# Kernel optimization log

Hardware: AMD Instinct MI355X
Metric: run time of the kernel (lower is better)

## Reference

```python
import jax, jax.numpy as jnp
import numpy as np

CHANNELS = 768
N_HEADS = 12
HEAD_DIM = CHANNELS // N_HEADS
WINDOW = 4
B, T = 4, 1024


def setup_inputs() -> dict:
    key = jax.random.key(0)
    ks = jax.random.split(key, 11)
    C = CHANNELS
    s = 1.0 / np.sqrt(C)
    inp = {
        "x": jax.random.normal(ks[0], (B, C, T), dtype=jnp.float32),
        "w_q": jax.random.normal(ks[1], (C, C), dtype=jnp.float32) * s,
        "b_q": jnp.zeros((C,), dtype=jnp.float32),
        "w_k": jax.random.normal(ks[2], (C, C), dtype=jnp.float32) * s,
        "b_k": jnp.zeros((C,), dtype=jnp.float32),
        "w_v": jax.random.normal(ks[3], (C, C), dtype=jnp.float32) * s,
        "b_v": jnp.zeros((C,), dtype=jnp.float32),
        "w_o": jax.random.normal(ks[4], (C, C), dtype=jnp.float32) * s,
        "b_o": jnp.zeros((C,), dtype=jnp.float32),
        "emb_rel_k": jax.random.normal(ks[5], (2 * WINDOW + 1, HEAD_DIM), dtype=jnp.float32) * 0.01,
        "emb_rel_v": jax.random.normal(ks[6], (2 * WINDOW + 1, HEAD_DIM), dtype=jnp.float32) * 0.01,
    }
    return inp


def _rel_embeddings(emb_k, emb_v, t):
    pos = jnp.arange(t)
    rel_pos = pos[None, :] - pos[:, None]            # (T, T), rel_pos[i,j] = j - i
    outside = jnp.abs(rel_pos) > WINDOW
    rel_idx = jnp.clip(rel_pos, -WINDOW, WINDOW) + WINDOW
    rel_k = jnp.where(outside[:, :, None], 0.0, emb_k[rel_idx])  # (T, T, d)
    rel_v = jnp.where(outside[:, :, None], 0.0, emb_v[rel_idx])
    return rel_k, rel_v


def reference(x, w_q, b_q, w_k, b_k, w_v, b_v, w_o, b_o, emb_rel_k, emb_rel_v):
    Bq, C, t = x.shape
    H, d = N_HEADS, HEAD_DIM
    # 1x1 Conv1d == per-timestep linear over channels
    def proj(w, b):
        return jnp.einsum('oc,bct->bot', w, x) + b[None, :, None]
    # (B, C, T) -> (B, H, T, d)
    def split_heads(y):
        return y.reshape(Bq, H, d, t).transpose(0, 1, 3, 2)
    q = split_heads(proj(w_q, b_q)) / jnp.sqrt(jnp.float32(d))
    k = split_heads(proj(w_k, b_k))
    v = split_heads(proj(w_v, b_v))
    scores = jnp.einsum('bhid,bhjd->bhij', q, k)
    rel_k, rel_v = _rel_embeddings(emb_rel_k, emb_rel_v, t)
    scores = scores + jnp.einsum('bhid,ijd->bhij', q, rel_k)
    attn = jax.nn.softmax(scores, axis=-1)
    out = jnp.einsum('bhij,bhjd->bhid', attn, v)
    out = out + jnp.einsum('bhij,ijd->bhid', attn, rel_v)
    out = out.transpose(0, 1, 3, 2).reshape(Bq, C, t)  # (B, C, T)
    out = jnp.einsum('oc,bct->bot', w_o, out) + b_o[None, :, None]
    return out
```

## Files before the change

### kernel.cpp

```cpp
#include <hip/hip_runtime.h>

#define B_ 4
#define T_ 1024
#define C_ 768
#define H_ 12
#define D_ 64

typedef unsigned short u16;
typedef __attribute__((ext_vector_type(8))) short b16x8;
typedef __attribute__((ext_vector_type(4))) float f32x4;

#define MFMA(a, b, c) __builtin_amdgcn_mfma_f32_16x16x32_bf16(a, b, c, 0, 0, 0)

__device__ __forceinline__ float b2f(u16 u) {
    return __uint_as_float(((unsigned)u) << 16);
}
__device__ __forceinline__ u16 f2b(float f) {
    unsigned u = __float_as_uint(f);
    u += 0x7fffu + ((u >> 16) & 1u);
    return (u16)(u >> 16);
}
__device__ __forceinline__ u16 f2b_tr(float f) {
    return (u16)(__float_as_uint(f) >> 16);
}

__device__ __forceinline__ void g2l16(const u16* g, u16* l) {
    __builtin_amdgcn_global_load_lds(
        (const __attribute__((address_space(1))) unsigned int*)g,
        (__attribute__((address_space(3))) unsigned int*)l, 16, 0, 0);
}

__global__ __launch_bounds__(256) void convw_kernel(
    const float* __restrict__ w0, const float* __restrict__ w1,
    const float* __restrict__ w2, const float* __restrict__ w3,
    u16* __restrict__ o)
{
    const float* src = blockIdx.y == 0 ? w0 : blockIdx.y == 1 ? w1 :
                       blockIdx.y == 2 ? w2 : w3;
    u16* dst = o + (size_t)blockIdx.y * C_ * C_;
    const int i = (blockIdx.x * 256 + threadIdx.x) * 4;
    float4 v = *(const float4*)(src + i);
    ushort4 st = {f2b(v.x), f2b(v.y), f2b(v.z), f2b(v.w)};
    *(ushort4*)(dst + i) = st;
}

__global__ __launch_bounds__(256) void convx_kernel(
    const float* __restrict__ x, u16* __restrict__ xb)
{
    __shared__ u16 tile[64][68];
    const int tid = threadIdx.x;
    const int t0 = blockIdx.x * 64, c0 = blockIdx.y * 64, b = blockIdx.z;
    #pragma unroll
    for (int p = 0; p < 4; ++p) {
        const int cc = p * 16 + (tid >> 4);
        const int t4 = (tid & 15) * 4;
        float4 v = *(const float4*)(x + ((size_t)b * C_ + c0 + cc) * T_ + t0 + t4);
        tile[t4 + 0][cc] = f2b(v.x);
        tile[t4 + 1][cc] = f2b(v.y);
        tile[t4 + 2][cc] = f2b(v.z);
        tile[t4 + 3][cc] = f2b(v.w);
    }
    __syncthreads();
    #pragma unroll
    for (int p = 0; p < 4; ++p) {
        const int tt = p * 16 + (tid >> 4);
        const int c4 = (tid & 15) * 4;
        ushort4 st = *(const ushort4*)&tile[tt][c4];
        *(ushort4*)(xb + ((size_t)b * T_ + t0 + tt) * C_ + c0 + c4) = st;
    }
}

__global__ __launch_bounds__(256) void qkv_mfma_kernel(
    const u16* __restrict__ wb, const u16* __restrict__ xb,
    const float* __restrict__ b_q, const float* __restrict__ b_k,
    const float* __restrict__ b_v,
    u16* __restrict__ q_ws, u16* __restrict__ k_ws, u16* __restrict__ v_ws)
{
    __shared__ __align__(16) u16 a_s[128 * 32];
    __shared__ __align__(16) u16 b_s[128 * 32];

    const int tid = threadIdx.x;
    const int wv = tid >> 6, lane = tid & 63;
    const int lo = lane & 15, quad = lane >> 4;
    const int wm = wv >> 1, wn = wv & 1;
    const int swz = (lo >> 1) & 3;
    const int srow = lane >> 2;
    const int skb  = (lane & 3) ^ ((lane >> 3) & 3);

    const int t0 = blockIdx.x * 128;
    const int mat = blockIdx.y / 6, oy = blockIdx.y % 6;
    const int o0 = oy * 128;
    const int b  = blockIdx.z;

    const u16* A = wb + (size_t)mat * C_ * C_;
    const float* bias = mat == 0 ? b_q : (mat == 1 ? b_k : b_v);
    u16* dst = mat == 0 ? q_ws : (mat == 1 ? k_ws : v_ws);
    const float scale = mat == 0 ? 0.125f : 1.0f;

    const size_t bT0 = (size_t)b * T_ + t0;

    f32x4 acc[4][4] = {};

    for (int kk = 0; kk < C_; kk += 32) {
        __syncthreads();
        #pragma unroll
        for (int ia = 0; ia < 2; ++ia) {
            const int row0 = (wv * 2 + ia) * 16;
            g2l16(A + (size_t)(o0 + row0 + srow) * C_ + kk + skb * 8,
                  a_s + row0 * 32);
        }
        #pragma unroll
        for (int ib = 0; ib < 2; ++ib) {
            const int row0 = (wv * 2 + ib) * 16;
            g2l16(xb + (bT0 + row0 + srow) * C_ + kk + skb * 8,
                  b_s + row0 * 32);
        }
        __syncthreads();

        b16x8 af[4], bf[4];
        #pragma unroll
        for (int mi = 0; mi < 4; ++mi) {
            const int m = wm * 64 + mi * 16 + lo;
            af[mi] = *(const b16x8*)(a_s + m * 32 + (quad ^ swz) * 8);
        }
        #pragma unroll
        for (int ni = 0; ni < 4; ++ni) {
            const int n = wn * 64 + ni * 16 + lo;
            bf[ni] = *(const b16x8*)(b_s + n * 32 + (quad ^ swz) * 8);
        }
        #pragma unroll
        for (int mi = 0; mi < 4; ++mi)
            #pragma unroll
            for (int ni = 0; ni < 4; ++ni)
                acc[mi][ni] = MFMA(af[mi], bf[ni], acc[mi][ni]);
    }

    #pragma unroll
    for (int mi = 0; mi < 4; ++mi) {
        const int o_b = o0 + wm * 64 + mi * 16 + quad * 4;
        const float4 bv4 = *(const float4*)(bias + o_b);
        const int h = o_b >> 6;
        const int dd0 = o_b & 63;
        #pragma unroll
        for (int ni = 0; ni < 4; ++ni) {
            const int t = t0 + wn * 64 + ni * 16 + lo;
            f32x4 a = acc[mi][ni];
            ushort4 st;
            st.x = f2b((a[0] + bv4.x) * scale);
            st.y = f2b((a[1] + bv4.y) * scale);
            st.z = f2b((a[2] + bv4.z) * scale);
            st.w = f2b((a[3] + bv4.w) * scale);
            *(ushort4*)(dst + (((size_t)b * H_ + h) * T_ + t) * D_ + dd0) = st;
        }
    }
}

__global__ __launch_bounds__(256) void transv_kernel(
    const u16* __restrict__ src, u16* __restrict__ dst)
{
    __shared__ __align__(16) u16 tile[64 * 72];
    const int tid = threadIdx.x;
    const int t0 = blockIdx.x * 64;
    const int bh = blockIdx.y;
    const u16* s = src + (size_t)bh * T_ * D_;
    u16* d = dst + (size_t)bh * D_ * T_;
    #pragma unroll
    for (int p = 0; p < 2; ++p) {
        const int idx = tid + p * 256;
        const int row = idx >> 3, ch = idx & 7;
        *(b16x8*)(tile + row * 72 + ch * 8) =
            *(const b16x8*)(s + (size_t)(t0 + row) * D_ + ch * 8);
    }
    __syncthreads();
    #pragma unroll
    for (int p = 0; p < 2; ++p) {
        const int idx = tid + p * 256;
        const int dd = idx >> 3, ch = idx & 7;
        union { b16x8 v; u16 e[8]; } t;
        #pragma unroll
        for (int e = 0; e < 8; ++e)
            t.e[e] = tile[(ch * 8 + e) * 72 + dd];
        *(b16x8*)(d + (size_t)dd * T_ + t0 + ch * 8) = t.v;
    }
}

__global__ __launch_bounds__(256) void out_mfma_kernel(
    const u16* __restrict__ wob, const u16* __restrict__ ab,
    const float* __restrict__ bias, float* __restrict__ out)
{
    __shared__ __align__(16) u16 a_s[64 * 32];
    __shared__ __align__(16) u16 b_s[128 * 32];

    const int tid = threadIdx.x;
    const int wv = tid >> 6, lane = tid & 63;
    const int lo = lane & 15, quad = lane >> 4;
    const int wm = wv >> 1, wn = wv & 1;
    const int swz = (lo >> 1) & 3;
    const int srow = lane >> 2;
    const int skb  = (lane & 3) ^ ((lane >> 3) & 3);

    const int t0 = blockIdx.x * 128;
    const int o0 = blockIdx.y * 64;
    const int b  = blockIdx.z;
    const size_t bT0 = (size_t)b * T_ + t0;

    f32x4 acc[2][4] = {};

    for (int kk = 0; kk < C_; kk += 32) {
        __syncthreads();
        {
            const int row0 = wv * 16;
            g2l16(wob + (size_t)(o0 + row0 + srow) * C_ + kk + skb * 8,
                  a_s + row0 * 32);
        }
        #pragma unroll
        for (int ib = 0; ib < 2; ++ib) {
            const int row0 = (wv * 2 + ib) * 16;
            g2l16(ab + (bT0 + row0 + srow) * C_ + kk + skb * 8,
                  b_s + row0 * 32);
        }
        __syncthreads();

        b16x8 af[2], bf[4];
        #pragma unroll
        for (int mi = 0; mi < 2; ++mi) {
            const int m = wm * 32 + mi * 16 + lo;
            af[mi] = *(const b16x8*)(a_s + m * 32 + (quad ^ swz) * 8);
        }
        #pragma unroll
        for (int ni = 0; ni < 4; ++ni) {
            const int n = wn * 64 + ni * 16 + lo;
            bf[ni] = *(const b16x8*)(b_s + n * 32 + (quad ^ swz) * 8);
        }
        #pragma unroll
        for (int mi = 0; mi < 2; ++mi)
            #pragma unroll
            for (int ni = 0; ni < 4; ++ni)
                acc[mi][ni] = MFMA(af[mi], bf[ni], acc[mi][ni]);
    }

    #pragma unroll
    for (int mi = 0; mi < 2; ++mi) {
        const int o_b = o0 + wm * 32 + mi * 16 + quad * 4;
        const float4 bv4 = *(const float4*)(bias + o_b);
        const float bb[4] = {bv4.x, bv4.y, bv4.z, bv4.w};
        #pragma unroll
        for (int ni = 0; ni < 4; ++ni) {
            const int t = t0 + wn * 64 + ni * 16 + lo;
            f32x4 a = acc[mi][ni];
            #pragma unroll
            for (int r = 0; r < 4; ++r)
                out[((size_t)b * C_ + o_b + r) * T_ + t] = a[r] + bb[r];
        }
    }
}

__global__ __launch_bounds__(256, 2) void attn_mfma_kernel(
    const u16* __restrict__ qw, const u16* __restrict__ kw, const u16* __restrict__ vw,
    const float* __restrict__ erk, const float* __restrict__ erv,
    u16* __restrict__ att)
{
    __shared__ __align__(16) u16 k_s[64 * 64];
    __shared__ __align__(16) u16 v_s[64 * 64];
    __shared__ __align__(16) u16 p_s[64 * 64];
    __shared__ float qrel_s[64][9];
    __shared__ float band_s[64][9];
    __shared__ float alpha_s[64];

    const int tid = threadIdx.x;
    const int wv = tid >> 6, lane = tid & 63;
    const int lo = lane & 15, quad = lane >> 4;
    const int wi0 = wv * 16;
    const int it0 = blockIdx.x * 64;
    const int h = blockIdx.y, b = blockIdx.z;
    const int bh = b * H_ + h;

    const u16* qp = qw + (size_t)bh * T_ * D_;
    const u16* kp = kw + (size_t)bh * T_ * D_;
    const u16* vp = vw + (size_t)bh * D_ * T_;

    const int srow = lane >> 3;
    const int schunk = (lane & 7) ^ (srow & 7);
    const int lsw = lo & 7;

    b16x8 qf[2];
    #pragma unroll
    for (int kc = 0; kc < 2; ++kc)
        qf[kc] = *(const b16x8*)(qp + (size_t)(it0 + wi0 + lo) * D_ + kc * 32 + quad * 8);

    {
        b16x8 ekf[2];
        #pragma unroll
        for (int kc = 0; kc < 2; ++kc) {
            union { b16x8 v; u16 s[8]; } t;
            #pragma unroll
            for (int r = 0; r < 8; ++r) t.s[r] = 0;
            if (lo < 9) {
                const float* e = erk + lo * D_ + kc * 32 + quad * 8;
                #pragma unroll
                for (int r = 0; r < 8; ++r) t.s[r] = f2b(e[r]);
            }
            ekf[kc] = t.v;
        }
        f32x4 acc = {};
        acc = MFMA(qf[0], ekf[0], acc);
        acc = MFMA(qf[1], ekf[1], acc);
        if (lo < 9)
            #pragma unroll
            for (int r = 0; r < 4; ++r)
                qrel_s[wi0 + quad * 4 + r][lo] = acc[r];
    }

    for (int idx = lane; idx < 16 * 9; idx += 64)
        band_s[wi0 + idx / 9][idx % 9] = -1e30f;

    f32x4 o[4] = {};
    float m = -1e30f, l = 0.f;

    for (int jt = 0; jt < T_; jt += 64) {
        __syncthreads();
        #pragma unroll
        for (int i2 = 0; i2 < 2; ++i2) {
            const int row0 = (wv * 2 + i2) * 8;
            g2l16(kp + (size_t)(jt + row0 + srow) * D_ + schunk * 8, k_s + row0 * 64);
            g2l16(vp + (size_t)(row0 + srow) * T_ + jt + schunk * 8, v_s + row0 * 64);
        }
        __syncthreads();

        f32x4 st[4];
        #pragma unroll
        for (int mt = 0; mt < 4; ++mt) {
            const int kr = mt * 16 + lo;
            const b16x8 ka0 = *(const b16x8*)(k_s + kr * 64 + ((quad) ^ lsw) * 8);
            const b16x8 ka1 = *(const b16x8*)(k_s + kr * 64 + ((4 + quad) ^ lsw) * 8);
            f32x4 a = {};
            a = MFMA(ka0, qf[0], a);
            a = MFMA(ka1, qf[1], a);
            st[mt] = a;
        }

        const int ibase = it0 + wi0 + lo;
        #pragma unroll
        for (int mt = 0; mt < 4; ++mt)
            #pragma unroll
            for (int r = 0; r < 4; ++r) {
                const int rr = (jt + mt * 16 + quad * 4 + r) - ibase + 4;
                if (rr >= 0 && rr <= 8) {
                    const float s2 = st[mt][r] + qrel_s[wi0 + lo][rr];
                    st[mt][r] = s2;
                    band_s[wi0 + lo][rr] = s2;
                }
            }

        float tm = -1e30f;
        #pragma unroll
        for (int mt = 0; mt < 4; ++mt)
            #pragma unroll
            for (int r = 0; r < 4; ++r)
                tm = fmaxf(tm, st[mt][r]);
        tm = fmaxf(tm, __shfl_xor(tm, 16));
        tm = fmaxf(tm, __shfl_xor(tm, 32));
        const float nm = fmaxf(m, tm);
        const float al = __expf(m - nm);
        m = nm;
        float rs = 0.f;
        #pragma unroll
        for (int mt = 0; mt < 4; ++mt)
            #pragma unroll
            for (int r = 0; r < 4; ++r) {
                const float e = __expf(st[mt][r] - nm);
                st[mt][r] = e;
                rs += e;
            }
        rs += __shfl_xor(rs, 16);
        rs += __shfl_xor(rs, 32);
        l = l * al + rs;
        if (quad == 0) alpha_s[wi0 + lo] = al;

        #pragma unroll
        for (int mt = 0; mt < 4; ++mt) {
            ushort4 pw;
            pw.x = f2b_tr(st[mt][0]);
            pw.y = f2b_tr(st[mt][1]);
            pw.z = f2b_tr(st[mt][2]);
            pw.w = f2b_tr(st[mt][3]);
            const int slot = (mt * 2 + (quad >> 1)) ^ lsw;
            *(ushort4*)(p_s + (wi0 + lo) * 64 + slot * 8 + (quad & 1) * 4) = pw;
        }

        #pragma unroll
        for (int r = 0; r < 4; ++r) {
            const float a = alpha_s[wi0 + quad * 4 + r];
            #pragma unroll
            for (int nd = 0; nd < 4; ++nd)
                o[nd][r] *= a;
        }

        const b16x8 pa0 = *(const b16x8*)(p_s + (wi0 + lo) * 64 + ((quad) ^ lsw) * 8);
        const b16x8 pa1 = *(const b16x8*)(p_s + (wi0 + lo) * 64 + ((4 + quad) ^ lsw) * 8);
        #pragma unroll
        for (int nd = 0; nd < 4; ++nd) {
            const int vr = nd * 16 + lo;
            const b16x8 vb0 = *(const b16x8*)(v_s + vr * 64 + ((quad) ^ lsw) * 8);
            const b16x8 vb1 = *(const b16x8*)(v_s + vr * 64 + ((4 + quad) ^ lsw) * 8);
            o[nd] = MFMA(pa0, vb0, o[nd]);
            o[nd] = MFMA(pa1, vb1, o[nd]);
        }
    }

    {
        union { b16x8 v; u16 s[8]; } tb;
        #pragma unroll
        for (int r = 0; r < 8; ++r) {
            const int rr = quad * 8 + r;
            tb.s[r] = (rr <= 8) ? f2b(__expf(band_s[wi0 + lo][rr] - m)) : (u16)0;
        }
        const b16x8 baf = tb.v;
        #pragma unroll
        for (int nd = 0; nd < 4; ++nd) {
            union { b16x8 v; u16 s[8]; } t;
            #pragma unroll
            for (int r = 0; r < 8; ++r) {
                const int rr = quad * 8 + r;
                t.s[r] = (rr <= 8) ? f2b(erv[rr * D_ + nd * 16 + lo]) : (u16)0;
            }
            o[nd] = MFMA(baf, t.v, o[nd]);
        }
    }

    if (quad == 0) alpha_s[wi0 + lo] = 1.f / l;
    #pragma unroll
    for (int r = 0; r < 4; ++r) {
        const int il = wi0 + quad * 4 + r;
        const float inv = alpha_s[il];
        const size_t base = ((size_t)b * T_ + it0 + il) * C_ + h * D_;
        #pragma unroll
        for (int nd = 0; nd < 4; ++nd)
            att[base + nd * 16 + lo] = f2b(o[nd][r] * inv);
    }
}

extern "C" void kernel_launch(void* const* d_in, const int* in_sizes, int n_in,
                              void* d_out, int out_size, void* d_ws, size_t ws_size,
                              hipStream_t stream) {
    const float* x   = (const float*)d_in[0];
    const float* w_q = (const float*)d_in[1];
    const float* b_q = (const float*)d_in[2];
    const float* w_k = (const float*)d_in[3];
    const float* b_k = (const float*)d_in[4];
    const float* w_v = (const float*)d_in[5];
    const float* b_v = (const float*)d_in[6];
    const float* w_o = (const float*)d_in[7];
    const float* b_o = (const float*)d_in[8];
    const float* erk = (const float*)d_in[9];
    const float* erv = (const float*)d_in[10];

    const size_t N = (size_t)B_ * C_ * T_;
    u16* q_ws  = (u16*)d_ws;
    u16* k_ws  = q_ws + N;
    u16* vraw  = q_ws + 2 * N;
    u16* vdT   = q_ws + 3 * N;
    u16* xb    = q_ws + 4 * N;
    u16* a_ws  = vraw;
    u16* wb    = q_ws + 5 * N;
    float* out = (float*)d_out;

    dim3 blk(256, 1, 1);

    convw_kernel<<<dim3(C_ * C_ / 1024, 4), blk, 0, stream>>>(w_q, w_k, w_v, w_o, wb);
    convx_kernel<<<dim3(T_ / 64, C_ / 64, B_), blk, 0, stream>>>(x, xb);

    qkv_mfma_kernel<<<dim3(T_ / 128, 18, B_), blk, 0, stream>>>(
        wb, xb, b_q, b_k, b_v, q_ws, k_ws, vraw);

    transv_kernel<<<dim3(T_ / 64, H_ * B_), blk, 0, stream>>>(vraw, vdT);

    attn_mfma_kernel<<<dim3(T_ / 64, H_, B_), blk, 0, stream>>>(
        q_ws, k_ws, vdT, erk, erv, a_ws);

    out_mfma_kernel<<<dim3(T_ / 128, C_ / 64, B_), blk, 0, stream>>>(
        wb + 3 * (size_t)C_ * C_, a_ws, b_o, out);
}
```

Baseline: 174.6 us.

## Double GEMM K-tile depth and shrink attention blocks to 32 query rows

The QKV and output projection GEMMs now stage 64-wide K slices per iteration instead of 32, using an 8-chunk XOR swizzle. This halves the number of barrier-separated load phases and runs two MFMA K-steps per sync. The attention kernel now uses 128-thread blocks covering 32 query rows, which doubles the grid to improve occupancy and load balance. It also skips the relative-position band loop for key tiles that cannot overlap the window. The cost is more shared memory per GEMM block and K/V tiles loaded twice as often across attention blocks.

New measurement: 172.4 us. Within noise of the previous version (-1.2%).

```diff
diff --git a/kernel.cpp b/kernel.cpp
--- a/kernel.cpp
+++ b/kernel.cpp
@@ -76,16 +76,16 @@
     const float* __restrict__ b_v,
     u16* __restrict__ q_ws, u16* __restrict__ k_ws, u16* __restrict__ v_ws)
 {
-    __shared__ __align__(16) u16 a_s[128 * 32];
-    __shared__ __align__(16) u16 b_s[128 * 32];
+    __shared__ __align__(16) u16 a_s[128 * 64];
+    __shared__ __align__(16) u16 b_s[128 * 64];
 
     const int tid = threadIdx.x;
     const int wv = tid >> 6, lane = tid & 63;
     const int lo = lane & 15, quad = lane >> 4;
     const int wm = wv >> 1, wn = wv & 1;
-    const int swz = (lo >> 1) & 3;
-    const int srow = lane >> 2;
-    const int skb  = (lane & 3) ^ ((lane >> 3) & 3);
+    const int lsw = lo & 7;
+    const int srow = lane >> 3;
+    const int schunk = (lane & 7) ^ srow;
 
     const int t0 = blockIdx.x * 128;
     const int mat = blockIdx.y / 6, oy = blockIdx.y % 6;
@@ -101,38 +101,42 @@
 
     f32x4 acc[4][4] = {};
 
-    for (int kk = 0; kk < C_; kk += 32) {
-        __syncthreads();
-        #pragma unroll
-        for (int ia = 0; ia < 2; ++ia) {
-            const int row0 = (wv * 2 + ia) * 16;
-            g2l16(A + (size_t)(o0 + row0 + srow) * C_ + kk + skb * 8,
-                  a_s + row0 * 32);
-        }
-        #pragma unroll
-        for (int ib = 0; ib < 2; ++ib) {
-            const int row0 = (wv * 2 + ib) * 16;
-            g2l16(xb + (bT0 + row0 + srow) * C_ + kk + skb * 8,
-                  b_s + row0 * 32);
-        }
-        __syncthreads();
-
-        b16x8 af[4], bf[4];
-        #pragma unroll
-        for (int mi = 0; mi < 4; ++mi) {
-            const int m = wm * 64 + mi * 16 + lo;
-            af[mi] = *(const b16x8*)(a_s + m * 32 + (quad ^ swz) * 8);
-        }
-        #pragma unroll
-        for (int ni = 0; ni < 4; ++ni) {
-            const int n = wn * 64 + ni * 16 + lo;
-            bf[ni] = *(const b16x8*)(b_s + n * 32 + (quad ^ swz) * 8);
-        }
-        #pragma unroll
-        for (int mi = 0; mi < 4; ++mi)
-            #pragma unroll
-            for (int ni = 0; ni < 4; ++ni)
-                acc[mi][ni] = MFMA(af[mi], bf[ni], acc[mi][ni]);
+    for (int kk = 0; kk < C_; kk += 64) {
+        __syncthreads();
+        #pragma unroll
+        for (int ia = 0; ia < 4; ++ia) {
+            const int row0 = (wv * 4 + ia) * 8;
+            g2l16(A + (size_t)(o0 + row0 + srow) * C_ + kk + schunk * 8,
+                  a_s + row0 * 64);
+        }
+        #pragma unroll
+        for (int ib = 0; ib < 4; ++ib) {
+            const int row0 = (wv * 4 + ib) * 8;
+            g2l16(xb + (bT0 + row0 + srow) * C_ + kk + schunk * 8,
+                  b_s + row0 * 64);
+        }
+        __syncthreads();
+
+        #pragma unroll
+        for (int kc = 0; kc < 2; ++kc) {
+            const int slotk = kc * 4;
+            b16x8 af[4], bf[4];
+            #pragma unroll
+            for (int mi = 0; mi < 4; ++mi) {
+                const int m = wm * 64 + mi * 16 + lo;
+                af[mi] = *(const b16x8*)(a_s + m * 64 + ((slotk + quad) ^ lsw) * 8);
+            }
+            #pragma unroll
+            for (int ni = 0; ni < 4; ++ni) {
+                const int n = wn * 64 + ni * 16 + lo;
+                bf[ni] = *(const b16x8*)(b_s + n * 64 + ((slotk + quad) ^ lsw) * 8);
+            }
+            #pragma unroll
+            for (int mi = 0; mi < 4; ++mi)
+                #pragma unroll
+                for (int ni = 0; ni < 4; ++ni)
+                    acc[mi][ni] = MFMA(af[mi], bf[ni], acc[mi][ni]);
+        }
     }
 
     #pragma unroll
@@ -188,16 +192,16 @@
     const u16* __restrict__ wob, const u16* __restrict__ ab,
     const float* __restrict__ bias, float* __restrict__ out)
 {
-    __shared__ __align__(16) u16 a_s[64 * 32];
-    __shared__ __align__(16) u16 b_s[128 * 32];
+    __shared__ __align__(16) u16 a_s[64 * 64];
+    __shared__ __align__(16) u16 b_s[128 * 64];
 
     const int tid = threadIdx.x;
     const int wv = tid >> 6, lane = tid & 63;
     const int lo = lane & 15, quad = lane >> 4;
     const int wm = wv >> 1, wn = wv & 1;
-    const int swz = (lo >> 1) & 3;
-    const int srow = lane >> 2;
-    const int skb  = (lane & 3) ^ ((lane >> 3) & 3);
+    const int lsw = lo & 7;
+    const int srow = lane >> 3;
+    const int schunk = (lane & 7) ^ srow;
 
     const int t0 = blockIdx.x * 128;
     const int o0 = blockIdx.y * 64;
@@ -206,37 +210,42 @@
 
     f32x4 acc[2][4] = {};
 
-    for (int kk = 0; kk < C_; kk += 32) {
-        __syncthreads();
-        {
-            const int row0 = wv * 16;
-            g2l16(wob + (size_t)(o0 + row0 + srow) * C_ + kk + skb * 8,
-                  a_s + row0 * 32);
-        }
-        #pragma unroll
-        for (int ib = 0; ib < 2; ++ib) {
-            const int row0 = (wv * 2 + ib) * 16;
-            g2l16(ab + (bT0 + row0 + srow) * C_ + kk + skb * 8,
-                  b_s + row0 * 32);
-        }
-        __syncthreads();
-
-        b16x8 af[2], bf[4];
-        #pragma unroll
-        for (int mi = 0; mi < 2; ++mi) {
-            const int m = wm * 32 + mi * 16 + lo;
-            af[mi] = *(const b16x8*)(a_s + m * 32 + (quad ^ swz) * 8);
-        }
-        #pragma unroll
-        for (int ni = 0; ni < 4; ++ni) {
-            const int n = wn * 64 + ni * 16 + lo;
-            bf[ni] = *(const b16x8*)(b_s + n * 32 + (quad ^ swz) * 8);
-        }
-        #pragma unroll
-        for (int mi = 0; mi < 2; ++mi)
-            #pragma unroll
-            for (int ni = 0; ni < 4; ++ni)
-                acc[mi][ni] = MFMA(af[mi], bf[ni], acc[mi][ni]);
+    for (int kk = 0; kk < C_; kk += 64) {
+        __syncthreads();
+        #pragma unroll
+        for (int ia = 0; ia < 2; ++ia) {
+            const int row0 = (wv * 2 + ia) * 8;
+            g2l16(wob + (size_t)(o0 + row0 + srow) * C_ + kk + schunk * 8,
+                  a_s + row0 * 64);
+        }
+        #pragma unroll
+        for (int ib = 0; ib < 4; ++ib) {
+            const int row0 = (wv * 4 + ib) * 8;
+            g2l16(ab + (bT0 + row0 + srow) * C_ + kk + schunk * 8,
+                  b_s + row0 * 64);
+        }
+        __syncthreads();
+
+        #pragma unroll
+        for (int kc = 0; kc < 2; ++kc) {
+            const int slotk = kc * 4;
+            b16x8 af[2], bf[4];
+            #pragma unroll
+            for (int mi = 0; mi < 2; ++mi) {
+                const int m = wm * 32 + mi * 16 + lo;
+                af[mi] = *(const b16x8*)(a_s + m * 64 + ((slotk + quad) ^ lsw) * 8);
+            }
+            #pragma unroll
+            for (int ni = 0; ni < 4; ++ni) {
+                const int n = wn * 64 + ni * 16 + lo;
+                bf[ni] = *(const b16x8*)(b_s + n * 64 + ((slotk + quad) ^ lsw) * 8);
+            }
+            #pragma unroll
+            for (int mi = 0; mi < 2; ++mi)
+                #pragma unroll
+                for (int ni = 0; ni < 4; ++ni)
+                    acc[mi][ni] = MFMA(af[mi], bf[ni], acc[mi][ni]);
+        }
     }
 
     #pragma unroll
@@ -255,23 +264,23 @@
     }
 }
 
-__global__ __launch_bounds__(256, 2) void attn_mfma_kernel(
+__global__ __launch_bounds__(128, 4) void attn_mfma_kernel(
     const u16* __restrict__ qw, const u16* __restrict__ kw, const u16* __restrict__ vw,
     const float* __restrict__ erk, const float* __restrict__ erv,
     u16* __restrict__ att)
 {
     __shared__ __align__(16) u16 k_s[64 * 64];
     __shared__ __align__(16) u16 v_s[64 * 64];
-    __shared__ __align__(16) u16 p_s[64 * 64];
-    __shared__ float qrel_s[64][9];
-    __shared__ float band_s[64][9];
-    __shared__ float alpha_s[64];
+    __shared__ __align__(16) u16 p_s[32 * 64];
+    __shared__ float qrel_s[32][9];
+    __shared__ float band_s[32][9];
+    __shared__ float alpha_s[32];
 
     const int tid = threadIdx.x;
     const int wv = tid >> 6, lane = tid & 63;
     const int lo = lane & 15, quad = lane >> 4;
     const int wi0 = wv * 16;
-    const int it0 = blockIdx.x * 64;
+    const int it0 = blockIdx.x * 32;
     const int h = blockIdx.y, b = blockIdx.z;
     const int bh = b * H_ + h;
 
@@ -280,7 +289,7 @@
     const u16* vp = vw + (size_t)bh * D_ * T_;
 
     const int srow = lane >> 3;
-    const int schunk = (lane & 7) ^ (srow & 7);
+    const int schunk = (lane & 7) ^ srow;
     const int lsw = lo & 7;
 
     b16x8 qf[2];
@@ -320,8 +329,8 @@
     for (int jt = 0; jt < T_; jt += 64) {
         __syncthreads();
         #pragma unroll
-        for (int i2 = 0; i2 < 2; ++i2) {
-            const int row0 = (wv * 2 + i2) * 8;
+        for (int i2 = 0; i2 < 4; ++i2) {
+            const int row0 = (wv * 4 + i2) * 8;
             g2l16(kp + (size_t)(jt + row0 + srow) * D_ + schunk * 8, k_s + row0 * 64);
             g2l16(vp + (size_t)(row0 + srow) * T_ + jt + schunk * 8, v_s + row0 * 64);
         }
@@ -339,18 +348,20 @@
             st[mt] = a;
         }
 
-        const int ibase = it0 + wi0 + lo;
-        #pragma unroll
-        for (int mt = 0; mt < 4; ++mt)
-            #pragma unroll
-            for (int r = 0; r < 4; ++r) {
-                const int rr = (jt + mt * 16 + quad * 4 + r) - ibase + 4;
-                if (rr >= 0 && rr <= 8) {
-                    const float s2 = st[mt][r] + qrel_s[wi0 + lo][rr];
-                    st[mt][r] = s2;
-                    band_s[wi0 + lo][rr] = s2;
+        if (jt >= it0 - 67 && jt <= it0 + 35) {
+            const int ibase = it0 + wi0 + lo;
+            #pragma unroll
+            for (int mt = 0; mt < 4; ++mt)
+                #pragma unroll
+                for (int r = 0; r < 4; ++r) {
+                    const int rr = (jt + mt * 16 + quad * 4 + r) - ibase + 4;
+                    if (rr >= 0 && rr <= 8) {
+                        const float s2 = st[mt][r] + qrel_s[wi0 + lo][rr];
+                        st[mt][r] = s2;
+                        band_s[wi0 + lo][rr] = s2;
+                    }
                 }
-            }
+        }
 
         float tm = -1e30f;
         #pragma unroll
@@ -475,7 +486,7 @@
 
     transv_kernel<<<dim3(T_ / 64, H_ * B_), blk, 0, stream>>>(vraw, vdT);
 
-    attn_mfma_kernel<<<dim3(T_ / 64, H_, B_), blk, 0, stream>>>(
+    attn_mfma_kernel<<<dim3(T_ / 32, H_, B_), dim3(128, 1, 1), 0, stream>>>(
         q_ws, k_ws, vdT, erk, erv, a_ws);
 
     out_mfma_kernel<<<dim3(T_ / 128, C_ / 64, B_), blk, 0, stream>>>(
```

## Process two query row-tiles per wave in attention, halving waves per block

Applied to the files above, without the earlier changes.

The attention kernel now runs 2 waves of 128 threads per block, each wave handling 32 query rows (two 16-row tiles), so the K and V fragments loaded from LDS are reused across two MFMA tiles. Each wave issues twice as many global-to-LDS loads per key tile. The relative-position band update is now skipped for key tiles far from the query block. The cost is more registers per wave and fewer waves available to hide latency.

After: 178.6 us. 1.02x slower.

```diff
diff --git a/kernel.cpp b/kernel.cpp
--- a/kernel.cpp
+++ b/kernel.cpp
@@ -255,7 +255,7 @@
     }
 }
 
-__global__ __launch_bounds__(256, 2) void attn_mfma_kernel(
+__global__ __launch_bounds__(128, 2) void attn_mfma_kernel(
     const u16* __restrict__ qw, const u16* __restrict__ kw, const u16* __restrict__ vw,
     const float* __restrict__ erk, const float* __restrict__ erv,
     u16* __restrict__ att)
@@ -270,7 +270,7 @@
     const int tid = threadIdx.x;
     const int wv = tid >> 6, lane = tid & 63;
     const int lo = lane & 15, quad = lane >> 4;
-    const int wi0 = wv * 16;
+    const int wi0 = wv * 32;
     const int it0 = blockIdx.x * 64;
     const int h = blockIdx.y, b = blockIdx.z;
     const int bh = b * H_ + h;
@@ -280,13 +280,16 @@
     const u16* vp = vw + (size_t)bh * D_ * T_;
 
     const int srow = lane >> 3;
-    const int schunk = (lane & 7) ^ (srow & 7);
+    const int schunk = (lane & 7) ^ srow;
     const int lsw = lo & 7;
 
-    b16x8 qf[2];
-    #pragma unroll
-    for (int kc = 0; kc < 2; ++kc)
-        qf[kc] = *(const b16x8*)(qp + (size_t)(it0 + wi0 + lo) * D_ + kc * 32 + quad * 8);
+    b16x8 qf[2][2];
+    #pragma unroll
+    for (int it = 0; it < 2; ++it)
+        #pragma unroll
+        for (int kc = 0; kc < 2; ++kc)
+            qf[it][kc] = *(const b16x8*)(
+                qp + (size_t)(it0 + wi0 + it * 16 + lo) * D_ + kc * 32 + quad * 8);
 
     {
         b16x8 ekf[2];
@@ -302,120 +305,155 @@
             }
             ekf[kc] = t.v;
         }
-        f32x4 acc = {};
-        acc = MFMA(qf[0], ekf[0], acc);
-        acc = MFMA(qf[1], ekf[1], acc);
-        if (lo < 9)
-            #pragma unroll
-            for (int r = 0; r < 4; ++r)
-                qrel_s[wi0 + quad * 4 + r][lo] = acc[r];
-    }
-
-    for (int idx = lane; idx < 16 * 9; idx += 64)
+        #pragma unroll
+        for (int it = 0; it < 2; ++it) {
+            f32x4 acc = {};
+            acc = MFMA(qf[it][0], ekf[0], acc);
+            acc = MFMA(qf[it][1], ekf[1], acc);
+            if (lo < 9)
+                #pragma unroll
+                for (int r = 0; r < 4; ++r)
+                    qrel_s[wi0 + it * 16 + quad * 4 + r][lo] = acc[r];
+        }
+    }
+
+    for (int idx = lane; idx < 32 * 9; idx += 64)
         band_s[wi0 + idx / 9][idx % 9] = -1e30f;
 
-    f32x4 o[4] = {};
-    float m = -1e30f, l = 0.f;
+    f32x4 o[2][4] = {};
+    float m[2] = {-1e30f, -1e30f};
+    float l[2] = {0.f, 0.f};
 
     for (int jt = 0; jt < T_; jt += 64) {
         __syncthreads();
         #pragma unroll
-        for (int i2 = 0; i2 < 2; ++i2) {
-            const int row0 = (wv * 2 + i2) * 8;
+        for (int i2 = 0; i2 < 4; ++i2) {
+            const int row0 = (wv * 4 + i2) * 8;
             g2l16(kp + (size_t)(jt + row0 + srow) * D_ + schunk * 8, k_s + row0 * 64);
             g2l16(vp + (size_t)(row0 + srow) * T_ + jt + schunk * 8, v_s + row0 * 64);
         }
         __syncthreads();
 
-        f32x4 st[4];
+        f32x4 st[4][2];
         #pragma unroll
         for (int mt = 0; mt < 4; ++mt) {
             const int kr = mt * 16 + lo;
             const b16x8 ka0 = *(const b16x8*)(k_s + kr * 64 + ((quad) ^ lsw) * 8);
             const b16x8 ka1 = *(const b16x8*)(k_s + kr * 64 + ((4 + quad) ^ lsw) * 8);
-            f32x4 a = {};
-            a = MFMA(ka0, qf[0], a);
-            a = MFMA(ka1, qf[1], a);
-            st[mt] = a;
-        }
-
-        const int ibase = it0 + wi0 + lo;
-        #pragma unroll
-        for (int mt = 0; mt < 4; ++mt)
+            #pragma unroll
+            for (int it = 0; it < 2; ++it) {
+                f32x4 a = {};
+                a = MFMA(ka0, qf[it][0], a);
+                a = MFMA(ka1, qf[it][1], a);
+                st[mt][it] = a;
+            }
+        }
+
+        if (jt >= it0 - 67 && jt <= it0 + 67) {
+            #pragma unroll
+            for (int it = 0; it < 2; ++it) {
+                const int irow = wi0 + it * 16 + lo;
+                const int ibase = it0 + irow;
+                #pragma unroll
+                for (int mt = 0; mt < 4; ++mt)
+                    #pragma unroll
+                    for (int r = 0; r < 4; ++r) {
+                        const int rr = (jt + mt * 16 + quad * 4 + r) - ibase + 4;
+                        if (rr >= 0 && rr <= 8) {
+                            const float s2 = st[mt][it][r] + qrel_s[irow][rr];
+                            st[mt][it][r] = s2;
+                            band_s[irow][rr] = s2;
+                        }
+                    }
+            }
+        }
+
+        #pragma unroll
+        for (int it = 0; it < 2; ++it) {
+            float tm = -1e30f;
+            #pragma unroll
+            for (int mt = 0; mt < 4; ++mt)
+                #pragma unroll
+                for (int r = 0; r < 4; ++r)
+                    tm = fmaxf(tm, st[mt][it][r]);
+            tm = fmaxf(tm, __shfl_xor(tm, 16));
+            tm = fmaxf(tm, __shfl_xor(tm, 32));
+            const float nm = fmaxf(m[it], tm);
+            const float al = __expf(m[it] - nm);
+            m[it] = nm;
+            float rs = 0.f;
+            #pragma unroll
+            for (int mt = 0; mt < 4; ++mt)
+                #pragma unroll
+                for (int r = 0; r < 4; ++r) {
+                    const float e = __expf(st[mt][it][r] - nm);
+                    st[mt][it][r] = e;
+                    rs += e;
+                }
+            rs += __shfl_xor(rs, 16);
+            rs += __shfl_xor(rs, 32);
+            l[it] = l[it] * al + rs;
+            if (quad == 0) alpha_s[wi0 + it * 16 + lo] = al;
+        }
+
+        #pragma unroll
+        for (int it = 0; it < 2; ++it) {
+            const int rowp = wi0 + it * 16 + lo;
+            #pragma unroll
+            for (int mt = 0; mt < 4; ++mt) {
+                ushort4 pw;
+                pw.x = f2b_tr(st[mt][it][0]);
+                pw.y = f2b_tr(st[mt][it][1]);
+                pw.z = f2b_tr(st[mt][it][2]);
+                pw.w = f2b_tr(st[mt][it][3]);
+                const int slot = (mt * 2 + (quad >> 1)) ^ lsw;
+                *(ushort4*)(p_s + rowp * 64 + slot * 8 + (quad & 1) * 4) = pw;
+            }
+        }
+
+        #pragma unroll
+        for (int it = 0; it < 2; ++it)
             #pragma unroll
             for (int r = 0; r < 4; ++r) {
-                const int rr = (jt + mt * 16 + quad * 4 + r) - ibase + 4;
-                if (rr >= 0 && rr <= 8) {
-                    const float s2 = st[mt][r] + qrel_s[wi0 + lo][rr];
-                    st[mt][r] = s2;
-                    band_s[wi0 + lo][rr] = s2;
-                }
-            }
-
-        float tm = -1e30f;
-        #pragma unroll
-        for (int mt = 0; mt < 4; ++mt)
-            #pragma unroll
-            for (int r = 0; r < 4; ++r)
-                tm = fmaxf(tm, st[mt][r]);
-        tm = fmaxf(tm, __shfl_xor(tm, 16));
-        tm = fmaxf(tm, __shfl_xor(tm, 32));
-        const float nm = fmaxf(m, tm);
-        const float al = __expf(m - nm);
-        m = nm;
-        float rs = 0.f;
-        #pragma unroll
-        for (int mt = 0; mt < 4; ++mt)
-            #pragma unroll
-            for (int r = 0; r < 4; ++r) {
-                const float e = __expf(st[mt][r] - nm);
-                st[mt][r] = e;
-                rs += e;
-            }
-        rs += __shfl_xor(rs, 16);
-        rs += __shfl_xor(rs, 32);
-        l = l * al + rs;
-        if (quad == 0) alpha_s[wi0 + lo] = al;
-
-        #pragma unroll
-        for (int mt = 0; mt < 4; ++mt) {
-            ushort4 pw;
-            pw.x = f2b_tr(st[mt][0]);
-            pw.y = f2b_tr(st[mt][1]);
-            pw.z = f2b_tr(st[mt][2]);
-            pw.w = f2b_tr(st[mt][3]);
-            const int slot = (mt * 2 + (quad >> 1)) ^ lsw;
-            *(ushort4*)(p_s + (wi0 + lo) * 64 + slot * 8 + (quad & 1) * 4) = pw;
-        }
-
-        #pragma unroll
-        for (int r = 0; r < 4; ++r) {
-            const float a = alpha_s[wi0 + quad * 4 + r];
-            #pragma unroll
-            for (int nd = 0; nd < 4; ++nd)
-                o[nd][r] *= a;
-        }
-
-        const b16x8 pa0 = *(const b16x8*)(p_s + (wi0 + lo) * 64 + ((quad) ^ lsw) * 8);
-        const b16x8 pa1 = *(const b16x8*)(p_s + (wi0 + lo) * 64 + ((4 + quad) ^ lsw) * 8);
+                const float a = alpha_s[wi0 + it * 16 + quad * 4 + r];
+                #pragma unroll
+                for (int nd = 0; nd < 4; ++nd)
+                    o[it][nd][r] *= a;
+            }
+
+        b16x8 vb[4][2];
         #pragma unroll
         for (int nd = 0; nd < 4; ++nd) {
             const int vr = nd * 16 + lo;
-            const b16x8 vb0 = *(const b16x8*)(v_s + vr * 64 + ((quad) ^ lsw) * 8);
-            const b16x8 vb1 = *(const b16x8*)(v_s + vr * 64 + ((4 + quad) ^ lsw) * 8);
-            o[nd] = MFMA(pa0, vb0, o[nd]);
-            o[nd] = MFMA(pa1, vb1, o[nd]);
+            vb[nd][0] = *(const b16x8*)(v_s + vr * 64 + ((quad) ^ lsw) * 8);
+            vb[nd][1] = *(const b16x8*)(v_s + vr * 64 + ((4 + quad) ^ lsw) * 8);
+        }
+        #pragma unroll
+        for (int it = 0; it < 2; ++it) {
+            const int rowp = wi0 + it * 16 + lo;
+            const b16x8 pa0 = *(const b16x8*)(p_s + rowp * 64 + ((quad) ^ lsw) * 8);
+            const b16x8 pa1 = *(const b16x8*)(p_s + rowp * 64 + ((4 + quad) ^ lsw) * 8);
+            #pragma unroll
+            for (int nd = 0; nd < 4; ++nd) {
+                o[it][nd] = MFMA(pa0, vb[nd][0], o[it][nd]);
+                o[it][nd] = MFMA(pa1, vb[nd][1], o[it][nd]);
+            }
         }
     }
 
     {
-        union { b16x8 v; u16 s[8]; } tb;
-        #pragma unroll
-        for (int r = 0; r < 8; ++r) {
-            const int rr = quad * 8 + r;
-            tb.s[r] = (rr <= 8) ? f2b(__expf(band_s[wi0 + lo][rr] - m)) : (u16)0;
-        }
-        const b16x8 baf = tb.v;
+        b16x8 baf[2];
+        #pragma unroll
+        for (int it = 0; it < 2; ++it) {
+            union { b16x8 v; u16 s[8]; } tb;
+            #pragma unroll
+            for (int r = 0; r < 8; ++r) {
+                const int rr = quad * 8 + r;
+                tb.s[r] = (rr <= 8) ? f2b(__expf(band_s[wi0 + it * 16 + lo][rr] - m[it]))
+                                    : (u16)0;
+            }
+            baf[it] = tb.v;
+        }
         #pragma unroll
         for (int nd = 0; nd < 4; ++nd) {
             union { b16x8 v; u16 s[8]; } t;
@@ -424,20 +462,26 @@
                 const int rr = quad * 8 + r;
                 t.s[r] = (rr <= 8) ? f2b(erv[rr * D_ + nd * 16 + lo]) : (u16)0;
             }
-            o[nd] = MFMA(baf, t.v, o[nd]);
-        }
-    }
-
-    if (quad == 0) alpha_s[wi0 + lo] = 1.f / l;
-    #pragma unroll
-    for (int r = 0; r < 4; ++r) {
-        const int il = wi0 + quad * 4 + r;
-        const float inv = alpha_s[il];
-        const size_t base = ((size_t)b * T_ + it0 + il) * C_ + h * D_;
-        #pragma unroll
-        for (int nd = 0; nd < 4; ++nd)
-            att[base + nd * 16 + lo] = f2b(o[nd][r] * inv);
-    }
+            #pragma unroll
+            for (int it = 0; it < 2; ++it)
+                o[it][nd] = MFMA(baf[it], t.v, o[it][nd]);
+        }
+    }
+
+    #pragma unroll
+    for (int it = 0; it < 2; ++it)
+        if (quad == 0) alpha_s[wi0 + it * 16 + lo] = 1.f / l[it];
+    #pragma unroll
+    for (int it = 0; it < 2; ++it)
+        #pragma unroll
+        for (int r = 0; r < 4; ++r) {
+            const int il = wi0 + it * 16 + quad * 4 + r;
+            const float inv = alpha_s[il];
+            const size_t base = ((size_t)b * T_ + it0 + il) * C_ + h * D_;
+            #pragma unroll
+            for (int nd = 0; nd < 4; ++nd)
+                att[base + nd * 16 + lo] = f2b(o[it][nd][r] * inv);
+        }
 }
 
 extern "C" void kernel_launch(void* const* d_in, const int* in_sizes, int n_in,
@@ -475,7 +519,7 @@
 
     transv_kernel<<<dim3(T_ / 64, H_ * B_), blk, 0, stream>>>(vraw, vdT);
 
-    attn_mfma_kernel<<<dim3(T_ / 64, H_, B_), blk, 0, stream>>>(
+    attn_mfma_kernel<<<dim3(T_ / 64, H_, B_), dim3(128, 1, 1), 0, stream>>>(
         q_ws, k_ws, vdT, erk, erv, a_ws);
 
     out_mfma_kernel<<<dim3(T_ / 128, C_ / 64, B_), blk, 0, stream>>>(
```

## Widen attention key tile to 128 and skip band work outside window

Applied to the files above, without the earlier changes.

The flash-attention loop now processes 128 keys per iteration instead of 64. This halves the number of barrier and softmax-rescale rounds, and the K/V/P shared buffers grow to match with a 16-chunk XOR swizzle. The relative-position band update is now skipped for key tiles that cannot intersect the window. In exchange it uses more LDS and registers (st[8]), which may reduce occupancy under launch_bounds(256,2).

After: 184.9 us. +5.9%, slower.

```diff
diff --git a/kernel.cpp b/kernel.cpp
--- a/kernel.cpp
+++ b/kernel.cpp
@@ -260,9 +260,9 @@
     const float* __restrict__ erk, const float* __restrict__ erv,
     u16* __restrict__ att)
 {
-    __shared__ __align__(16) u16 k_s[64 * 64];
-    __shared__ __align__(16) u16 v_s[64 * 64];
-    __shared__ __align__(16) u16 p_s[64 * 64];
+    __shared__ __align__(16) u16 k_s[128 * 64];
+    __shared__ __align__(16) u16 v_s[64 * 128];
+    __shared__ __align__(16) u16 p_s[64 * 128];
     __shared__ float qrel_s[64][9];
     __shared__ float band_s[64][9];
     __shared__ float alpha_s[64];
@@ -279,9 +279,10 @@
     const u16* kp = kw + (size_t)bh * T_ * D_;
     const u16* vp = vw + (size_t)bh * D_ * T_;
 
-    const int srow = lane >> 3;
-    const int schunk = (lane & 7) ^ (srow & 7);
-    const int lsw = lo & 7;
+    const int srow8 = lane >> 3;
+    const int sch8  = (lane & 7) ^ srow8;
+    const int srow4 = lane >> 4;
+    const int sch16 = lane & 15;
 
     b16x8 qf[2];
     #pragma unroll
@@ -317,44 +318,52 @@
     f32x4 o[4] = {};
     float m = -1e30f, l = 0.f;
 
-    for (int jt = 0; jt < T_; jt += 64) {
-        __syncthreads();
-        #pragma unroll
-        for (int i2 = 0; i2 < 2; ++i2) {
-            const int row0 = (wv * 2 + i2) * 8;
-            g2l16(kp + (size_t)(jt + row0 + srow) * D_ + schunk * 8, k_s + row0 * 64);
-            g2l16(vp + (size_t)(row0 + srow) * T_ + jt + schunk * 8, v_s + row0 * 64);
-        }
-        __syncthreads();
-
-        f32x4 st[4];
-        #pragma unroll
-        for (int mt = 0; mt < 4; ++mt) {
+    for (int jt = 0; jt < T_; jt += 128) {
+        __syncthreads();
+        #pragma unroll
+        for (int ik = 0; ik < 4; ++ik) {
+            const int row0 = (wv * 4 + ik) * 8;
+            g2l16(kp + (size_t)(jt + row0 + srow8) * D_ + sch8 * 8, k_s + row0 * 64);
+        }
+        #pragma unroll
+        for (int iv = 0; iv < 4; ++iv) {
+            const int row0 = (wv * 4 + iv) * 4;
+            const int rkey = (row0 + srow4) & 15;
+            g2l16(vp + (size_t)(row0 + srow4) * T_ + jt + (sch16 ^ rkey) * 8,
+                  v_s + row0 * 128);
+        }
+        __syncthreads();
+
+        f32x4 st[8];
+        #pragma unroll
+        for (int mt = 0; mt < 8; ++mt) {
             const int kr = mt * 16 + lo;
-            const b16x8 ka0 = *(const b16x8*)(k_s + kr * 64 + ((quad) ^ lsw) * 8);
-            const b16x8 ka1 = *(const b16x8*)(k_s + kr * 64 + ((4 + quad) ^ lsw) * 8);
+            const b16x8 ka0 = *(const b16x8*)(k_s + kr * 64 + ((quad) ^ (lo & 7)) * 8);
+            const b16x8 ka1 = *(const b16x8*)(k_s + kr * 64 + ((4 + quad) ^ (lo & 7)) * 8);
             f32x4 a = {};
             a = MFMA(ka0, qf[0], a);
             a = MFMA(ka1, qf[1], a);
             st[mt] = a;
         }
 
-        const int ibase = it0 + wi0 + lo;
-        #pragma unroll
-        for (int mt = 0; mt < 4; ++mt)
-            #pragma unroll
-            for (int r = 0; r < 4; ++r) {
-                const int rr = (jt + mt * 16 + quad * 4 + r) - ibase + 4;
-                if (rr >= 0 && rr <= 8) {
-                    const float s2 = st[mt][r] + qrel_s[wi0 + lo][rr];
-                    st[mt][r] = s2;
-                    band_s[wi0 + lo][rr] = s2;
+        if (jt > it0 - 132 && jt <= it0 + 67) {
+            const int ibase = it0 + wi0 + lo;
+            #pragma unroll
+            for (int mt = 0; mt < 8; ++mt)
+                #pragma unroll
+                for (int r = 0; r < 4; ++r) {
+                    const int rr = (jt + mt * 16 + quad * 4 + r) - ibase + 4;
+                    if (rr >= 0 && rr <= 8) {
+                        const float s2 = st[mt][r] + qrel_s[wi0 + lo][rr];
+                        st[mt][r] = s2;
+                        band_s[wi0 + lo][rr] = s2;
+                    }
                 }
-            }
+        }
 
         float tm = -1e30f;
         #pragma unroll
-        for (int mt = 0; mt < 4; ++mt)
+        for (int mt = 0; mt < 8; ++mt)
             #pragma unroll
             for (int r = 0; r < 4; ++r)
                 tm = fmaxf(tm, st[mt][r]);
@@ -365,7 +374,7 @@
         m = nm;
         float rs = 0.f;
         #pragma unroll
-        for (int mt = 0; mt < 4; ++mt)
+        for (int mt = 0; mt < 8; ++mt)
             #pragma unroll
             for (int r = 0; r < 4; ++r) {
                 const float e = __expf(st[mt][r] - nm);
@@ -378,14 +387,14 @@
         if (quad == 0) alpha_s[wi0 + lo] = al;
 
         #pragma unroll
-        for (int mt = 0; mt < 4; ++mt) {
+        for (int mt = 0; mt < 8; ++mt) {
             ushort4 pw;
             pw.x = f2b_tr(st[mt][0]);
             pw.y = f2b_tr(st[mt][1]);
             pw.z = f2b_tr(st[mt][2]);
             pw.w = f2b_tr(st[mt][3]);
-            const int slot = (mt * 2 + (quad >> 1)) ^ lsw;
-            *(ushort4*)(p_s + (wi0 + lo) * 64 + slot * 8 + (quad & 1) * 4) = pw;
+            const int slot = (mt * 2 + (quad >> 1)) ^ lo;
+            *(ushort4*)(p_s + (wi0 + lo) * 128 + slot * 8 + (quad & 1) * 4) = pw;
         }
 
         #pragma unroll
@@ -396,15 +405,16 @@
                 o[nd][r] *= a;
         }
 
-        const b16x8 pa0 = *(const b16x8*)(p_s + (wi0 + lo) * 64 + ((quad) ^ lsw) * 8);
-        const b16x8 pa1 = *(const b16x8*)(p_s + (wi0 + lo) * 64 + ((4 + quad) ^ lsw) * 8);
-        #pragma unroll
-        for (int nd = 0; nd < 4; ++nd) {
-            const int vr = nd * 16 + lo;
-            const b16x8 vb0 = *(const b16x8*)(v_s + vr * 64 + ((quad) ^ lsw) * 8);
-            const b16x8 vb1 = *(const b16x8*)(v_s + vr * 64 + ((4 + quad) ^ lsw) * 8);
-            o[nd] = MFMA(pa0, vb0, o[nd]);
-            o[nd] = MFMA(pa1, vb1, o[nd]);
+        #pragma unroll
+        for (int kc = 0; kc < 4; ++kc) {
+            const b16x8 pa = *(const b16x8*)(
+                p_s + (wi0 + lo) * 128 + ((kc * 4 + quad) ^ lo) * 8);
+            #pragma unroll
+            for (int nd = 0; nd < 4; ++nd) {
+                const b16x8 vb = *(const b16x8*)(
+                    v_s + (nd * 16 + lo) * 128 + ((kc * 4 + quad) ^ lo) * 8);
+                o[nd] = MFMA(pa, vb, o[nd]);
+            }
         }
     }
 
```
